# Kernel optimization log

Hardware: AMD Instinct MI355X
Metric: run time of the kernel (lower is better)

## Reference

```python
import jax, jax.numpy as jnp
import numpy as np

DIM = 128
N_VARS = 2048
N_CLAUSES = 8192
N_ROUNDS = 26
ADJ_DENSITY = 0.0015  # ~6 literals per clause


def setup_inputs() -> dict:
    key = jax.random.key(0)
    ks = iter(jax.random.split(key, 40))

    def w(shape):
        fan_in = shape[-1]
        return jax.random.normal(next(ks), shape, jnp.float32) / jnp.sqrt(jnp.float32(fan_in))

    def b(shape):
        return jax.random.normal(next(ks), shape, jnp.float32) * 0.05

    adj = (jax.random.uniform(next(ks), (2 * N_VARS, N_CLAUSES)) < ADJ_DENSITY).astype(jnp.float32)
    inp = {
        'adj': adj,
        'l_init_w': w((DIM, 1)), 'l_init_b': b((DIM,)),
        'c_init_w': w((DIM, 1)), 'c_init_b': b((DIM,)),
        'lmsg_w1': w((DIM, DIM)), 'lmsg_b1': b((DIM,)),
        'lmsg_w2': w((DIM, DIM)), 'lmsg_b2': b((DIM,)),
        'lmsg_w3': w((DIM, DIM)), 'lmsg_b3': b((DIM,)),
        'cmsg_w1': w((DIM, DIM)), 'cmsg_b1': b((DIM,)),
        'cmsg_w2': w((DIM, DIM)), 'cmsg_b2': b((DIM,)),
        'cmsg_w3': w((DIM, DIM)), 'cmsg_b3': b((DIM,)),
        'l_wih': w((4 * DIM, 2 * DIM)), 'l_whh': w((4 * DIM, DIM)),
        'l_bih': b((4 * DIM,)), 'l_bhh': b((4 * DIM,)),
        'c_wih': w((4 * DIM, DIM)), 'c_whh': w((4 * DIM, DIM)),
        'c_bih': b((4 * DIM,)), 'c_bhh': b((4 * DIM,)),
        'lvote_w1': w((DIM, DIM)), 'lvote_b1': b((DIM,)),
        'lvote_w2': w((DIM, DIM)), 'lvote_b2': b((DIM,)),
        'lvote_w3': w((1, DIM)), 'lvote_b3': b((1,)),
    }
    return inp


def _mlp(x, w1, b1, w2, b2, w3, b3):
    x = jax.nn.relu(x @ w1.T + b1)
    x = jax.nn.relu(x @ w2.T + b2)
    return x @ w3.T + b3


def _lstm_step(x, h, c, wih, whh, bih, bhh):
    # torch.nn.LSTM gate order: i, f, g, o
    g = x @ wih.T + h @ whh.T + bih + bhh
    i, f, gg, o = jnp.split(g, 4, axis=-1)
    c = jax.nn.sigmoid(f) * c + jax.nn.sigmoid(i) * jnp.tanh(gg)
    h = jax.nn.sigmoid(o) * jnp.tanh(c)
    return h, c


def reference(adj, l_init_w, l_init_b, c_init_w, c_init_b,
              lmsg_w1, lmsg_b1, lmsg_w2, lmsg_b2, lmsg_w3, lmsg_b3,
              cmsg_w1, cmsg_b1, cmsg_w2, cmsg_b2, cmsg_w3, cmsg_b3,
              l_wih, l_whh, l_bih, l_bhh,
              c_wih, c_whh, c_bih, c_bhh,
              lvote_w1, lvote_b1, lvote_w2, lvote_b2, lvote_w3, lvote_b3):
    n_lits, n_clauses = adj.shape
    n_vars = n_lits // 2
    dim = l_init_b.shape[0]

    # L_init / C_init: Linear(1,dim) applied to ones(1), tiled across rows
    Lh = jnp.broadcast_to(l_init_w[:, 0] + l_init_b, (n_lits, dim))
    Ch = jnp.broadcast_to(c_init_w[:, 0] + c_init_b, (n_clauses, dim))
    Lc = jnp.zeros((n_lits, dim), jnp.float32)
    Cc = jnp.zeros((n_clauses, dim), jnp.float32)

    def step(carry, _):
        Lh, Lc, Ch, Cc = carry
        L_pre = _mlp(Lh, lmsg_w1, lmsg_b1, lmsg_w2, lmsg_b2, lmsg_w3, lmsg_b3)
        LC_msg = adj.T @ L_pre                       # [n_clauses, dim]
        Ch, Cc = _lstm_step(LC_msg, Ch, Cc, c_wih, c_whh, c_bih, c_bhh)
        C_pre = _mlp(Ch, cmsg_w1, cmsg_b1, cmsg_w2, cmsg_b2, cmsg_w3, cmsg_b3)
        CL_msg = adj @ C_pre                         # [2*n_vars, dim]
        L_flip = jnp.concatenate([Lh[n_vars:], Lh[:n_vars]], axis=0)
        x = jnp.concatenate([CL_msg, L_flip], axis=1)  # [2*n_vars, 2*dim]
        Lh, Lc = _lstm_step(x, Lh, Lc, l_wih, l_whh, l_bih, l_bhh)
        return (Lh, Lc, Ch, Cc), None

    (Lh, Lc, Ch, Cc), _ = jax.lax.scan(step, (Lh, Lc, Ch, Cc), None, length=N_ROUNDS)

    logits = Lh
    vote = _mlp(logits, lvote_w1, lvote_b1, lvote_w2, lvote_b2, lvote_w3, lvote_b3)  # [2*n_vars, 1]
    vote_join = jnp.concatenate([vote[:n_vars], vote[n_vars:]], axis=1)  # [n_vars, 2]
    vote_mean = jnp.mean(vote_join)[None]  # single problem in batch -> [1]
    return vote_mean, vote, logits
```

## Files before the change

### kernel.cpp

```cpp
#include <hip/hip_runtime.h>
#include <math.h>

#define NL 4096
#define NV 2048
#define NC 8192
#define DIM 128
#define NG 512
#define NROUNDS 26

#define CSEG 64
#define CSEGLEN 64
#define CSEGCAP 8
#define LSEG 32
#define LSEGLEN 256
#define LSEGCAP 16
#define CCAP 32
#define LCAP 48

__device__ __forceinline__ float sigf(float x){ return 1.0f/(1.0f+expf(-x)); }

__global__ void k_transpose(const float* __restrict__ src, float* __restrict__ dst,
                            int R, int C){
  __shared__ float t[32][33];
  int cb = blockIdx.x*32, rb = blockIdx.y*32;
  int x = threadIdx.x, y = threadIdx.y;
  for (int i = y; i < 32; i += 8){
    int r = rb+i, c = cb+x;
    if (r < R && c < C) t[i][x] = src[(size_t)r*C + c];
  }
  __syncthreads();
  for (int i = y; i < 32; i += 8){
    int c = cb+i, r = rb+x;
    if (c < C && r < R) dst[(size_t)c*R + r] = t[x][i];
  }
}

__global__ void k_permq(const float* __restrict__ W, int K,
                        float* __restrict__ dst, int koff){
  int idx = blockIdx.x*blockDim.x + threadIdx.x;
  if (idx >= K*NG) return;
  int k = idx >> 9, j = idx & (NG-1);
  int g = j & 3, d = j >> 2;
  dst[(size_t)(koff+k)*NG + j] = W[(size_t)(g*DIM+d)*K + k];
}

__global__ void k_permb(const float* __restrict__ bih, const float* __restrict__ bhh,
                        float* __restrict__ bq){
  int j = blockIdx.x*blockDim.x + threadIdx.x;
  if (j >= NG) return;
  int g = j & 3, d = j >> 2;
  bq[j] = bih[g*DIM+d] + bhh[g*DIM+d];
}

__global__ void k_build_cseg(const float* __restrict__ adj,
                             int* __restrict__ scnt, int* __restrict__ slst){
  int idx = blockIdx.x*blockDim.x + threadIdx.x;
  int c4 = idx & (NC/4 - 1);
  int s  = idx >> 11;
  if (s >= CSEG) return;
  int base = s*CSEGLEN;
  int c0 = c4*4;
  int n0=0, n1=0, n2=0, n3=0;
  for (int i = 0; i < CSEGLEN; ++i){
    float4 v = *(const float4*)&adj[(size_t)(base+i)*NC + c0];
    if (v.x != 0.f){ if (n0 < CSEGCAP) slst[((size_t)(c0+0)*CSEG + s)*CSEGCAP + n0] = base+i; ++n0; }
    if (v.y != 0.f){ if (n1 < CSEGCAP) slst[((size_t)(c0+1)*CSEG + s)*CSEGCAP + n1] = base+i; ++n1; }
    if (v.z != 0.f){ if (n2 < CSEGCAP) slst[((size_t)(c0+2)*CSEG + s)*CSEGCAP + n2] = base+i; ++n2; }
    if (v.w != 0.f){ if (n3 < CSEGCAP) slst[((size_t)(c0+3)*CSEG + s)*CSEGCAP + n3] = base+i; ++n3; }
  }
  scnt[(c0+0)*CSEG + s] = n0 < CSEGCAP ? n0 : CSEGCAP;
  scnt[(c0+1)*CSEG + s] = n1 < CSEGCAP ? n1 : CSEGCAP;
  scnt[(c0+2)*CSEG + s] = n2 < CSEGCAP ? n2 : CSEGCAP;
  scnt[(c0+3)*CSEG + s] = n3 < CSEGCAP ? n3 : CSEGCAP;
}

__global__ void k_build_lseg(const float* __restrict__ adj,
                             int* __restrict__ scnt, int* __restrict__ slst){
  int gtid = blockIdx.x*blockDim.x + threadIdx.x;
  int wid  = gtid >> 6;
  int lane = threadIdx.x & 63;
  int l = wid >> 5;
  int s = wid & (LSEG-1);
  if (l >= NL) return;
  int base = s*LSEGLEN;
  int c0 = base + lane*4;
  float4 v = *(const float4*)&adj[(size_t)l*NC + c0];
  float vv[4] = {v.x, v.y, v.z, v.w};
  unsigned long long below = (lane == 0) ? 0ull : ((1ull<<lane)-1ull);
  int* out = slst + ((size_t)l*LSEG + s)*LSEGCAP;
  unsigned long long m[4];
  int nb = 0;
#pragma unroll
  for (int j = 0; j < 4; ++j){
    m[j] = __ballot(vv[j] != 0.f);
    nb += __popcll(m[j] & below);
  }
  int myoff = 0;
#pragma unroll
  for (int j = 0; j < 4; ++j){
    if (vv[j] != 0.f){
      int pos = nb + myoff;
      if (pos < LSEGCAP) out[pos] = c0 + j;
      ++myoff;
    }
  }
  if (lane == 0){
    int tot = 0;
#pragma unroll
    for (int j = 0; j < 4; ++j) tot += __popcll(m[j]);
    scnt[l*LSEG+s] = tot < LSEGCAP ? tot : LSEGCAP;
  }
}

__global__ void k_merge_c(const int* __restrict__ scnt, const int* __restrict__ slst,
                          int* __restrict__ cnt, int* __restrict__ lst){
  int c = blockIdx.x*blockDim.x + threadIdx.x;
  if (c >= NC) return;
  int n = 0;
  for (int s = 0; s < CSEG; ++s){
    int m = scnt[c*CSEG+s];
    const int* in = slst + ((size_t)c*CSEG+s)*CSEGCAP;
    for (int t = 0; t < m; ++t){ if (n < CCAP) lst[(size_t)c*CCAP+n] = in[t]; ++n; }
  }
  cnt[c] = n < CCAP ? n : CCAP;
}

__global__ void k_merge_l(const int* __restrict__ scnt, const int* __restrict__ slst,
                          int* __restrict__ cnt, int* __restrict__ lst){
  int l = blockIdx.x*blockDim.x + threadIdx.x;
  if (l >= NL) return;
  int n = 0;
  for (int s = 0; s < LSEG; ++s){
    int m = scnt[l*LSEG+s];
    const int* in = slst + ((size_t)l*LSEG+s)*LSEGCAP;
    for (int t = 0; t < m; ++t){ if (n < LCAP) lst[(size_t)l*LCAP+n] = in[t]; ++n; }
  }
  cnt[l] = n < LCAP ? n : LCAP;
}

__global__ void k_init(const float* __restrict__ liw, const float* __restrict__ lib,
                       const float* __restrict__ ciw, const float* __restrict__ cib,
                       float* __restrict__ Lh, float* __restrict__ Lc,
                       float* __restrict__ Ch, float* __restrict__ Cc){
  int idx = blockIdx.x*blockDim.x + threadIdx.x;
  int d = idx & (DIM-1);
  if (idx < NL*DIM){ Lh[idx] = liw[d] + lib[d]; Lc[idx] = 0.0f; }
  if (idx < NC*DIM){ Ch[idx] = ciw[d] + cib[d]; Cc[idx] = 0.0f; }
}

template<int CAP>
__global__ __launch_bounds__(256)
void k_gather(const float* __restrict__ X,
              const int* __restrict__ cnt, const int* __restrict__ lst,
              float* __restrict__ out){
  int tid = threadIdx.x;
  int r = blockIdx.x*8 + (tid>>5);
  int q = tid & 31;
  float4 s = make_float4(0.f,0.f,0.f,0.f);
  int n = cnt[r];
  const int* ls = lst + (size_t)r*CAP;
  for (int e = 0; e < n; ++e){
    float4 u = *(const float4*)&X[(size_t)ls[e]*DIM + q*4];
    s.x += u.x; s.y += u.y; s.z += u.z; s.w += u.w;
  }
  *(float4*)&out[(size_t)r*DIM + q*4] = s;
}

template<int ASRC, int BN>
__global__ __launch_bounds__(256)
void k_lstm(const float* __restrict__ Xmsg,
            const float* __restrict__ Hin,
            const float* __restrict__ Wq, const float* __restrict__ bq,
            float* __restrict__ Cst, float* __restrict__ Hout){
  constexpr int KT  = (ASRC==1) ? 256 : 384;
  constexpr int NT  = KT/16;
  constexpr int TN  = BN/16;
  constexpr int BQ  = BN/4;
  constexpr int NBS = (16*BQ)/256;
  __shared__ __align__(16) float As[16][68];
  __shared__ __align__(16) float4 Bs4[16*BQ];
  int tid = threadIdx.x;
  int tx = tid & 15, ty = tid >> 4;
  int m0 = blockIdx.x*64, n0 = blockIdx.y*BN;
  int arow = tid >> 2, akq = tid & 3;
  int grow = m0 + arow;
  int frow = (grow + NV) & (NL-1);

  float acc[4][TN];
#pragma unroll
  for (int r = 0; r < 4; ++r)
#pragma unroll
    for (int c = 0; c < TN; ++c) acc[r][c] = 0.f;

  for (int t = 0; t < NT; ++t){
    int k0 = t*16;
    const float* ap;
    if (ASRC == 1){
      ap = (k0 < 128) ? &Xmsg[(size_t)grow*DIM + k0]
                      : &Hin[(size_t)grow*DIM + (k0-128)];
    } else {
      ap = (k0 < 128) ? &Xmsg[(size_t)grow*DIM + k0]
         : (k0 < 256) ? &Hin[(size_t)frow*DIM + (k0-128)]
                      : &Hin[(size_t)grow*DIM + (k0-256)];
    }
    float4 av = *(const float4*)(ap + akq*4);
    float4 bv[NBS];
#pragma unroll
    for (int i = 0; i < NBS; ++i){
      int s = tid + i*256;
      int bk = s / BQ, bc = s % BQ;
      bv[i] = *(const float4*)&Wq[(size_t)(k0+bk)*NG + n0 + bc*4];
    }
    __syncthreads();
    As[akq*4+0][arow] = av.x;
    As[akq*4+1][arow] = av.y;
    As[akq*4+2][arow] = av.z;
    As[akq*4+3][arow] = av.w;
#pragma unroll
    for (int i = 0; i < NBS; ++i){
      int s = tid + i*256;
      int bk = s / BQ, bc = s % BQ;
      if (BN == 128) Bs4[(bk*2 + (bc&1))*16 + (bc>>1)] = bv[i];
      else           Bs4[bk*16 + bc] = bv[i];
    }
    __syncthreads();
#pragma unroll
    for (int k = 0; k < 16; ++k){
      float4 a = *(const float4*)&As[k][ty*4];
      float ar[4] = {a.x, a.y, a.z, a.w};
      if (TN == 8){
        float4 b0 = Bs4[(k*2+0)*16 + tx];
        float4 b1 = Bs4[(k*2+1)*16 + tx];
        float br[8] = {b0.x,b0.y,b0.z,b0.w,b1.x,b1.y,b1.z,b1.w};
#pragma unroll
        for (int r = 0; r < 4; ++r)
#pragma unroll
          for (int c = 0; c < 8; ++c) acc[r][c] += ar[r]*br[c];
      } else {
        float4 b0 = Bs4[k*16 + tx];
        float br[4] = {b0.x,b0.y,b0.z,b0.w};
#pragma unroll
        for (int r = 0; r < 4; ++r)
#pragma unroll
          for (int c = 0; c < 4; ++c) acc[r][c] += ar[r]*br[c];
      }
    }
  }

  if (TN == 8){
    float4 bq0 = *(const float4*)&bq[n0 + tx*8];
    float4 bq1 = *(const float4*)&bq[n0 + tx*8 + 4];
    int d0 = (n0 >> 2) + tx*2;
#pragma unroll
    for (int rr = 0; rr < 4; ++rr){
      int row = m0 + ty*4 + rr;
      float2 c = *(const float2*)&Cst[(size_t)row*DIM + d0];
      float i0 = acc[rr][0]+bq0.x, f0 = acc[rr][1]+bq0.y;
      float g0 = acc[rr][2]+bq0.z, o0 = acc[rr][3]+bq0.w;
      float i1 = acc[rr][4]+bq1.x, f1 = acc[rr][5]+bq1.y;
      float g1 = acc[rr][6]+bq1.z, o1 = acc[rr][7]+bq1.w;
      float cn0 = sigf(f0)*c.x + sigf(i0)*tanhf(g0);
      float cn1 = sigf(f1)*c.y + sigf(i1)*tanhf(g1);
      float hn0 = sigf(o0)*tanhf(cn0);
      float hn1 = sigf(o1)*tanhf(cn1);
      *(float2*)&Cst[(size_t)row*DIM + d0]  = make_float2(cn0, cn1);
      *(float2*)&Hout[(size_t)row*DIM + d0] = make_float2(hn0, hn1);
    }
  } else {
    float4 bqv = *(const float4*)&bq[n0 + tx*4];
    int d = (n0 >> 2) + tx;
#pragma unroll
    for (int rr = 0; rr < 4; ++rr){
      int row = m0 + ty*4 + rr;
      float c = Cst[(size_t)row*DIM + d];
      float ig = acc[rr][0]+bqv.x, fg = acc[rr][1]+bqv.y;
      float gg = acc[rr][2]+bqv.z, og = acc[rr][3]+bqv.w;
      float cn = sigf(fg)*c + sigf(ig)*tanhf(gg);
      float hn = sigf(og)*tanhf(cn);
      Cst[(size_t)row*DIM + d]  = cn;
      Hout[(size_t)row*DIM + d] = hn;
    }
  }
}

template<int BM>
__global__ __launch_bounds__(256)
void k_mlp3r(const float* __restrict__ in, float* __restrict__ out,
             const float* __restrict__ w1, const float* __restrict__ b1,
             const float* __restrict__ w2, const float* __restrict__ b2,
             const float* __restrict__ w3, const float* __restrict__ b3){
  constexpr int TM = BM/8;
  __shared__ __align__(16) float xs[BM][132];
  __shared__ __align__(16) float4 Bs4[512];
  int tid = threadIdx.x;
  int tx = tid & 31, ty = tid >> 5;
  int m0 = blockIdx.x*BM;
#pragma unroll
  for (int i = 0; i < BM/8; ++i){
    int idx = tid + i*256;
    int row = idx >> 5, c4 = idx & 31;
    *(float4*)&xs[row][c4*4] = *(const float4*)&in[(size_t)(m0+row)*DIM + c4*4];
  }
  const float* W[3] = {w1, w2, w3};
  const float* B[3] = {b1, b2, b3};
#pragma unroll
  for (int l = 0; l < 3; ++l){
    float acc[TM][4];
#pragma unroll
    for (int r = 0; r < TM; ++r)
#pragma unroll
      for (int c = 0; c < 4; ++c) acc[r][c] = 0.f;
    for (int kt = 0; kt < 8; ++kt){
      float4 wv0, wv1;
      { int s = tid;      wv0 = *(const float4*)&W[l][(size_t)(kt*16+(s>>5))*DIM + (s&31)*4]; }
      { int s = tid+256;  wv1 = *(const float4*)&W[l][(size_t)(kt*16+(s>>5))*DIM + (s&31)*4]; }
      __syncthreads();
      { int s = tid;      Bs4[(s>>5)*32 + (s&31)] = wv0; }
      { int s = tid+256;  Bs4[(s>>5)*32 + (s&31)] = wv1; }
      __syncthreads();
#pragma unroll
      for (int k4 = 0; k4 < 4; ++k4){
        float4 a[TM];
#pragma unroll
        for (int r = 0; r < TM; ++r)
          a[r] = *(const float4*)&xs[ty*TM+r][kt*16 + k4*4];
#pragma unroll
        for (int kk = 0; kk < 4; ++kk){
          float4 b = Bs4[(k4*4+kk)*32 + tx];
          float br[4] = {b.x, b.y, b.z, b.w};
#pragma unroll
          for (int r = 0; r < TM; ++r){
            float av = (kk==0) ? a[r].x : (kk==1) ? a[r].y : (kk==2) ? a[r].z : a[r].w;
#pragma unroll
            for (int c = 0; c < 4; ++c) acc[r][c] += av*br[c];
          }
        }
      }
    }
    float4 bb = *(const float4*)&B[l][tx*4];
    if (l < 2){
      __syncthreads();
#pragma unroll
      for (int r = 0; r < TM; ++r){
        float4 v = make_float4(fmaxf(acc[r][0]+bb.x, 0.f), fmaxf(acc[r][1]+bb.y, 0.f),
                               fmaxf(acc[r][2]+bb.z, 0.f), fmaxf(acc[r][3]+bb.w, 0.f));
        *(float4*)&xs[ty*TM+r][tx*4] = v;
      }
    } else {
#pragma unroll
      for (int r = 0; r < TM; ++r){
        int row = m0 + ty*TM + r;
        float4 v = make_float4(acc[r][0]+bb.x, acc[r][1]+bb.y,
                               acc[r][2]+bb.z, acc[r][3]+bb.w);
        *(float4*)&out[(size_t)row*DIM + tx*4] = v;
      }
    }
  }
}

template<bool RELU>
__device__ __forceinline__ void mlp_layer8v(const float (*__restrict__ xs)[DIM],
                                            float (*__restrict__ ys)[DIM],
                                            const float* __restrict__ Wt,
                                            const float* __restrict__ B, int tid){
  int j4 = (tid & 31)*4, slot = tid >> 5;
  float a0=0.f, a1=0.f, a2=0.f, a3=0.f;
#pragma unroll 4
  for (int k = 0; k < DIM; k += 4){
    float4 w0 = *(const float4*)&Wt[(size_t)(k+0)*DIM + j4];
    float4 w1 = *(const float4*)&Wt[(size_t)(k+1)*DIM + j4];
    float4 w2 = *(const float4*)&Wt[(size_t)(k+2)*DIM + j4];
    float4 w3 = *(const float4*)&Wt[(size_t)(k+3)*DIM + j4];
    float4 x  = *(const float4*)&xs[slot][k];
    a0 += x.x*w0.x + x.y*w1.x + x.z*w2.x + x.w*w3.x;
    a1 += x.x*w0.y + x.y*w1.y + x.z*w2.y + x.w*w3.y;
    a2 += x.x*w0.z + x.y*w1.z + x.z*w2.z + x.w*w3.z;
    a3 += x.x*w0.w + x.y*w1.w + x.z*w2.w + x.w*w3.w;
  }
  float4 b = *(const float4*)&B[j4];
  float4 v = make_float4(a0+b.x, a1+b.y, a2+b.z, a3+b.w);
  if (RELU){
    v.x = fmaxf(v.x,0.f); v.y = fmaxf(v.y,0.f);
    v.z = fmaxf(v.z,0.f); v.w = fmaxf(v.w,0.f);
  }
  *(float4*)&ys[slot][j4] = v;
}

__global__ __launch_bounds__(256, 4)
void k_vote(const float* __restrict__ Lh, float* __restrict__ vote,
            float* __restrict__ dout,
            const float* __restrict__ w1t, const float* __restrict__ b1,
            const float* __restrict__ w2t, const float* __restrict__ b2,
            const float* __restrict__ w3, const float* __restrict__ b3){
  __shared__ __align__(16) float xs[8][DIM];
  __shared__ __align__(16) float ys[8][DIM];
  int r0 = blockIdx.x*8;
  int tid = threadIdx.x;
  {
    int row = tid >> 5, c4 = (tid & 31)*4;
    float4 v = *(const float4*)&Lh[(size_t)(r0+row)*DIM + c4];
    *(float4*)&xs[row][c4] = v;
    *(float4*)&dout[1 + NL + (size_t)(r0+row)*DIM + c4] = v;
  }
  __syncthreads();
  mlp_layer8v<true>(xs, ys, w1t, b1, tid);
  __syncthreads();
  mlp_layer8v<true>(ys, xs, w2t, b2, tid);
  __syncthreads();
  int r = tid >> 5, lane32 = tid & 31;
  float4 x = *(const float4*)&xs[r][lane32*4];
  float4 w = *(const float4*)&w3[lane32*4];
  float pp = x.x*w.x + x.y*w.y + x.z*w.z + x.w*w.w;
  pp += __shfl_down(pp, 16, 32);
  pp += __shfl_down(pp, 8, 32);
  pp += __shfl_down(pp, 4, 32);
  pp += __shfl_down(pp, 2, 32);
  pp += __shfl_down(pp, 1, 32);
  if (lane32 == 0){
    float t = pp + b3[0];
    vote[r0+r] = t;
    dout[1 + r0 + r] = t;
  }
}

__global__ void k_mean(const float* __restrict__ vote, float* __restrict__ dout){
  __shared__ float red[256];
  int tid = threadIdx.x;
  float s = 0.f;
  for (int i = tid; i < NL; i += 256) s += vote[i];
  red[tid] = s;
  __syncthreads();
  for (int w = 128; w > 0; w >>= 1){
    if (tid < w) red[tid] += red[tid+w];
    __syncthreads();
  }
  if (tid == 0) dout[0] = red[0] / (float)NL;
}

static inline void launch_transpose(const float* src, float* dst, int R, int C,
                                    hipStream_t stream){
  dim3 g((C+31)/32, (R+31)/32), b(32, 8);
  k_transpose<<<g, b, 0, stream>>>(src, dst, R, C);
}

extern "C" void kernel_launch(void* const* d_in, const int* in_sizes, int n_in,
                              void* d_out, int out_size, void* d_ws, size_t ws_size,
                              hipStream_t stream){
  const float* adj      = (const float*)d_in[0];
  const float* l_init_w = (const float*)d_in[1];
  const float* l_init_b = (const float*)d_in[2];
  const float* c_init_w = (const float*)d_in[3];
  const float* c_init_b = (const float*)d_in[4];
  const float* lmsg_w1  = (const float*)d_in[5];
  const float* lmsg_b1  = (const float*)d_in[6];
  const float* lmsg_w2  = (const float*)d_in[7];
  const float* lmsg_b2  = (const float*)d_in[8];
  const float* lmsg_w3  = (const float*)d_in[9];
  const float* lmsg_b3  = (const float*)d_in[10];
  const float* cmsg_w1  = (const float*)d_in[11];
  const float* cmsg_b1  = (const float*)d_in[12];
  const float* cmsg_w2  = (const float*)d_in[13];
  const float* cmsg_b2  = (const float*)d_in[14];
  const float* cmsg_w3  = (const float*)d_in[15];
  const float* cmsg_b3  = (const float*)d_in[16];
  const float* l_wih    = (const float*)d_in[17];
  const float* l_whh    = (const float*)d_in[18];
  const float* l_bih    = (const float*)d_in[19];
  const float* l_bhh    = (const float*)d_in[20];
  const float* c_wih    = (const float*)d_in[21];
  const float* c_whh    = (const float*)d_in[22];
  const float* c_bih    = (const float*)d_in[23];
  const float* c_bhh    = (const float*)d_in[24];
  const float* lvote_w1 = (const float*)d_in[25];
  const float* lvote_b1 = (const float*)d_in[26];
  const float* lvote_w2 = (const float*)d_in[27];
  const float* lvote_b2 = (const float*)d_in[28];
  const float* lvote_w3 = (const float*)d_in[29];
  const float* lvote_b3 = (const float*)d_in[30];

  char* p = (char*)d_ws;
  auto alloc = [&](size_t bytes) -> void* {
    void* r = (void*)p;
    p += (bytes + 255) & ~(size_t)255;
    return r;
  };
  float* LhA   = (float*)alloc((size_t)NL*DIM*4);
  float* LhB   = (float*)alloc((size_t)NL*DIM*4);
  float* Lc    = (float*)alloc((size_t)NL*DIM*4);
  float* ChA   = (float*)alloc((size_t)NC*DIM*4);
  float* Cc    = (float*)alloc((size_t)NC*DIM*4);
  float* vote  = (float*)alloc((size_t)NL*4);
  int* ccnt    = (int*)alloc((size_t)NC*4);
  int* clst    = (int*)alloc((size_t)NC*CCAP*4);
  int* lcnt    = (int*)alloc((size_t)NL*4);
  int* llst    = (int*)alloc((size_t)NL*LCAP*4);
  float* lm1t  = (float*)alloc((size_t)DIM*DIM*4);
  float* lm2t  = (float*)alloc((size_t)DIM*DIM*4);
  float* lm3t  = (float*)alloc((size_t)DIM*DIM*4);
  float* cm1t  = (float*)alloc((size_t)DIM*DIM*4);
  float* cm2t  = (float*)alloc((size_t)DIM*DIM*4);
  float* cm3t  = (float*)alloc((size_t)DIM*DIM*4);
  float* vw1t  = (float*)alloc((size_t)DIM*DIM*4);
  float* vw2t  = (float*)alloc((size_t)DIM*DIM*4);
  float* WqC   = (float*)alloc((size_t)256*NG*4);
  float* WqL   = (float*)alloc((size_t)384*NG*4);
  float* bqC   = (float*)alloc((size_t)NG*4);
  float* bqL   = (float*)alloc((size_t)NG*4);
  char* scratch = (char*)alloc((size_t)28*1024*1024);
  int* scnt_c  = (int*)scratch;
  int* slst_c  = (int*)(scratch + (size_t)NC*CSEG*4);
  int* scnt_l  = (int*)(scratch + (size_t)(NC*CSEG + NC*CSEG*CSEGCAP)*4);
  int* slst_l  = (int*)(scratch + (size_t)(NC*CSEG + NC*CSEG*CSEGCAP + NL*LSEG)*4);
  float* ChB   = (float*)(scratch);
  float* Cpre  = (float*)(scratch + (size_t)4*1024*1024);
  float* Lpre  = (float*)(scratch + (size_t)8*1024*1024);
  float* Cmsg  = (float*)(scratch + (size_t)10*1024*1024);
  float* Lmsg  = (float*)(scratch + (size_t)14*1024*1024);
  (void)ws_size; (void)in_sizes; (void)n_in; (void)out_size;

  launch_transpose(lmsg_w1, lm1t, DIM, DIM, stream);
  launch_transpose(lmsg_w2, lm2t, DIM, DIM, stream);
  launch_transpose(lmsg_w3, lm3t, DIM, DIM, stream);
  launch_transpose(cmsg_w1, cm1t, DIM, DIM, stream);
  launch_transpose(cmsg_w2, cm2t, DIM, DIM, stream);
  launch_transpose(cmsg_w3, cm3t, DIM, DIM, stream);
  launch_transpose(lvote_w1, vw1t, DIM, DIM, stream);
  launch_transpose(lvote_w2, vw2t, DIM, DIM, stream);
  k_permq<<<(128*NG)/256, 256, 0, stream>>>(c_wih, 128, WqC, 0);
  k_permq<<<(128*NG)/256, 256, 0, stream>>>(c_whh, 128, WqC, 128);
  k_permq<<<(256*NG)/256, 256, 0, stream>>>(l_wih, 256, WqL, 0);
  k_permq<<<(128*NG)/256, 256, 0, stream>>>(l_whh, 128, WqL, 256);
  k_permb<<<NG/256, 256, 0, stream>>>(c_bih, c_bhh, bqC);
  k_permb<<<NG/256, 256, 0, stream>>>(l_bih, l_bhh, bqL);

  k_build_cseg<<<(NC/4)*CSEG/256, 256, 0, stream>>>(adj, scnt_c, slst_c);
  k_build_lseg<<<NL*LSEG*64/256, 256, 0, stream>>>(adj, scnt_l, slst_l);
  k_merge_c<<<NC/256, 256, 0, stream>>>(scnt_c, slst_c, ccnt, clst);
  k_merge_l<<<NL/256, 256, 0, stream>>>(scnt_l, slst_l, lcnt, llst);
  k_init<<<NC*DIM/256, 256, 0, stream>>>(l_init_w, l_init_b, c_init_w, c_init_b,
                                         LhA, Lc, ChA, Cc);

  float* Lh_cur = LhA; float* Lh_nxt = LhB;
  float* Ch_cur = ChA; float* Ch_nxt = ChB;

  k_mlp3r<8><<<NL/8, 256, 0, stream>>>(Lh_cur, Lpre,
                                       lm1t, lmsg_b1, lm2t, lmsg_b2, lm3t, lmsg_b3);
  for (int r = 0; r < NROUNDS; ++r){
    k_gather<CCAP><<<NC/8, 256, 0, stream>>>(Lpre, ccnt, clst, Cmsg);
    k_lstm<1,64><<<dim3(NC/64, 8), 256, 0, stream>>>(Cmsg, Ch_cur, WqC, bqC, Cc, Ch_nxt);
    k_mlp3r<8><<<NC/8, 256, 0, stream>>>(Ch_nxt, Cpre,
                                         cm1t, cmsg_b1, cm2t, cmsg_b2, cm3t, cmsg_b3);
    k_gather<LCAP><<<NL/8, 256, 0, stream>>>(Cpre, lcnt, llst, Lmsg);
    k_lstm<2,64><<<dim3(NL/64, 8), 256, 0, stream>>>(Lmsg, Lh_cur, WqL, bqL, Lc, Lh_nxt);
    k_mlp3r<8><<<NL/8, 256, 0, stream>>>(Lh_nxt, Lpre,
                                         lm1t, lmsg_b1, lm2t, lmsg_b2, lm3t, lmsg_b3);
    float* t;
    t = Lh_cur; Lh_cur = Lh_nxt; Lh_nxt = t;
    t = Ch_cur; Ch_cur = Ch_nxt; Ch_nxt = t;
  }

  k_vote<<<NL/8, 256, 0, stream>>>(Lh_cur, vote, (float*)d_out,
                                   vw1t, lvote_b1, vw2t, lvote_b2,
                                   lvote_w3, lvote_b3);
  k_mean<<<1, 256, 0, stream>>>(vote, (float*)d_out);
}
```

Before: 3.588 ms.

## Fuse sparse neighbor gather into LSTM GEMM kernel prologue

Removes the separate gather kernels and writes the aggregated message rows straight into shared memory at the start of each LSTM GEMM block. The first 128 K-columns then read from that shared tile instead of a global message buffer. This cuts two launches per round and the global write and read of the message tensors. In exchange, each of the 8 column blocks (grid y) repeats the same gather, so sparse reads grow eightfold, and the larger shared tile may reduce occupancy.

```diff
diff --git a/kernel.cpp b/kernel.cpp
--- a/kernel.cpp
+++ b/kernel.cpp
@@ -148,138 +148,104 @@
   if (idx < NC*DIM){ Ch[idx] = ciw[d] + cib[d]; Cc[idx] = 0.0f; }
 }
 
-template<int CAP>
+template<int ASRC>
 __global__ __launch_bounds__(256)
-void k_gather(const float* __restrict__ X,
-              const int* __restrict__ cnt, const int* __restrict__ lst,
-              float* __restrict__ out){
-  int tid = threadIdx.x;
-  int r = blockIdx.x*8 + (tid>>5);
-  int q = tid & 31;
-  float4 s = make_float4(0.f,0.f,0.f,0.f);
-  int n = cnt[r];
-  const int* ls = lst + (size_t)r*CAP;
-  for (int e = 0; e < n; ++e){
-    float4 u = *(const float4*)&X[(size_t)ls[e]*DIM + q*4];
-    s.x += u.x; s.y += u.y; s.z += u.z; s.w += u.w;
-  }
-  *(float4*)&out[(size_t)r*DIM + q*4] = s;
-}
-
-template<int ASRC, int BN>
-__global__ __launch_bounds__(256)
-void k_lstm(const float* __restrict__ Xmsg,
+void k_lstm(const float* __restrict__ Xg,
+            const int* __restrict__ cnt, const int* __restrict__ lst,
             const float* __restrict__ Hin,
             const float* __restrict__ Wq, const float* __restrict__ bq,
             float* __restrict__ Cst, float* __restrict__ Hout){
   constexpr int KT  = (ASRC==1) ? 256 : 384;
   constexpr int NT  = KT/16;
-  constexpr int TN  = BN/16;
-  constexpr int BQ  = BN/4;
-  constexpr int NBS = (16*BQ)/256;
+  constexpr int LCP = (ASRC==1) ? CCAP : LCAP;
+  __shared__ __align__(16) float Am[DIM][68];
   __shared__ __align__(16) float As[16][68];
-  __shared__ __align__(16) float4 Bs4[16*BQ];
+  __shared__ __align__(16) float4 Bs4[16*16];
   int tid = threadIdx.x;
   int tx = tid & 15, ty = tid >> 4;
-  int m0 = blockIdx.x*64, n0 = blockIdx.y*BN;
+  int m0 = blockIdx.x*64, n0 = blockIdx.y*64;
   int arow = tid >> 2, akq = tid & 3;
   int grow = m0 + arow;
   int frow = (grow + NV) & (NL-1);
 
-  float acc[4][TN];
+  {
+    int n = cnt[grow];
+    const int* ls = lst + (size_t)grow*LCP;
+    float4 g[8];
+#pragma unroll
+    for (int j = 0; j < 8; ++j) g[j] = make_float4(0.f,0.f,0.f,0.f);
+    for (int e = 0; e < n; ++e){
+      const float* xr = &Xg[(size_t)ls[e]*DIM];
+#pragma unroll
+      for (int j = 0; j < 8; ++j){
+        float4 u = *(const float4*)&xr[(akq + 4*j)*4];
+        g[j].x += u.x; g[j].y += u.y; g[j].z += u.z; g[j].w += u.w;
+      }
+    }
+#pragma unroll
+    for (int j = 0; j < 8; ++j){
+      int k0 = (akq + 4*j)*4;
+      Am[k0+0][arow] = g[j].x;
+      Am[k0+1][arow] = g[j].y;
+      Am[k0+2][arow] = g[j].z;
+      Am[k0+3][arow] = g[j].w;
+    }
+  }
+  __syncthreads();
+
+  float acc[4][4];
 #pragma unroll
   for (int r = 0; r < 4; ++r)
 #pragma unroll
-    for (int c = 0; c < TN; ++c) acc[r][c] = 0.f;
+    for (int c = 0; c < 4; ++c) acc[r][c] = 0.f;
 
   for (int t = 0; t < NT; ++t){
     int k0 = t*16;
-    const float* ap;
-    if (ASRC == 1){
-      ap = (k0 < 128) ? &Xmsg[(size_t)grow*DIM + k0]
-                      : &Hin[(size_t)grow*DIM + (k0-128)];
+    float4 bv = *(const float4*)&Wq[(size_t)(k0 + (tid>>4))*NG + n0 + (tid&15)*4];
+    if (t >= 8){
+      const float* ap;
+      if (ASRC == 1)       ap = &Hin[(size_t)grow*DIM + (k0-128)];
+      else if (k0 < 256)   ap = &Hin[(size_t)frow*DIM + (k0-128)];
+      else                 ap = &Hin[(size_t)grow*DIM + (k0-256)];
+      float4 av = *(const float4*)(ap + akq*4);
+      __syncthreads();
+      As[akq*4+0][arow] = av.x;
+      As[akq*4+1][arow] = av.y;
+      As[akq*4+2][arow] = av.z;
+      As[akq*4+3][arow] = av.w;
+      Bs4[(tid>>4)*16 + (tid&15)] = bv;
+      __syncthreads();
     } else {
-      ap = (k0 < 128) ? &Xmsg[(size_t)grow*DIM + k0]
-         : (k0 < 256) ? &Hin[(size_t)frow*DIM + (k0-128)]
-                      : &Hin[(size_t)grow*DIM + (k0-256)];
-    }
-    float4 av = *(const float4*)(ap + akq*4);
-    float4 bv[NBS];
-#pragma unroll
-    for (int i = 0; i < NBS; ++i){
-      int s = tid + i*256;
-      int bk = s / BQ, bc = s % BQ;
-      bv[i] = *(const float4*)&Wq[(size_t)(k0+bk)*NG + n0 + bc*4];
-    }
-    __syncthreads();
-    As[akq*4+0][arow] = av.x;
-    As[akq*4+1][arow] = av.y;
-    As[akq*4+2][arow] = av.z;
-    As[akq*4+3][arow] = av.w;
-#pragma unroll
-    for (int i = 0; i < NBS; ++i){
-      int s = tid + i*256;
-      int bk = s / BQ, bc = s % BQ;
-      if (BN == 128) Bs4[(bk*2 + (bc&1))*16 + (bc>>1)] = bv[i];
-      else           Bs4[bk*16 + bc] = bv[i];
-    }
-    __syncthreads();
+      __syncthreads();
+      Bs4[(tid>>4)*16 + (tid&15)] = bv;
+      __syncthreads();
+    }
 #pragma unroll
     for (int k = 0; k < 16; ++k){
-      float4 a = *(const float4*)&As[k][ty*4];
+      float4 a = (t < 8) ? *(const float4*)&Am[k0+k][ty*4]
+                         : *(const float4*)&As[k][ty*4];
       float ar[4] = {a.x, a.y, a.z, a.w};
-      if (TN == 8){
-        float4 b0 = Bs4[(k*2+0)*16 + tx];
-        float4 b1 = Bs4[(k*2+1)*16 + tx];
-        float br[8] = {b0.x,b0.y,b0.z,b0.w,b1.x,b1.y,b1.z,b1.w};
-#pragma unroll
-        for (int r = 0; r < 4; ++r)
-#pragma unroll
-          for (int c = 0; c < 8; ++c) acc[r][c] += ar[r]*br[c];
-      } else {
-        float4 b0 = Bs4[k*16 + tx];
-        float br[4] = {b0.x,b0.y,b0.z,b0.w};
-#pragma unroll
-        for (int r = 0; r < 4; ++r)
-#pragma unroll
-          for (int c = 0; c < 4; ++c) acc[r][c] += ar[r]*br[c];
-      }
-    }
-  }
-
-  if (TN == 8){
-    float4 bq0 = *(const float4*)&bq[n0 + tx*8];
-    float4 bq1 = *(const float4*)&bq[n0 + tx*8 + 4];
-    int d0 = (n0 >> 2) + tx*2;
-#pragma unroll
-    for (int rr = 0; rr < 4; ++rr){
-      int row = m0 + ty*4 + rr;
-      float2 c = *(const float2*)&Cst[(size_t)row*DIM + d0];
-      float i0 = acc[rr][0]+bq0.x, f0 = acc[rr][1]+bq0.y;
-      float g0 = acc[rr][2]+bq0.z, o0 = acc[rr][3]+bq0.w;
-      float i1 = acc[rr][4]+bq1.x, f1 = acc[rr][5]+bq1.y;
-      float g1 = acc[rr][6]+bq1.z, o1 = acc[rr][7]+bq1.w;
-      float cn0 = sigf(f0)*c.x + sigf(i0)*tanhf(g0);
-      float cn1 = sigf(f1)*c.y + sigf(i1)*tanhf(g1);
-      float hn0 = sigf(o0)*tanhf(cn0);
-      float hn1 = sigf(o1)*tanhf(cn1);
-      *(float2*)&Cst[(size_t)row*DIM + d0]  = make_float2(cn0, cn1);
-      *(float2*)&Hout[(size_t)row*DIM + d0] = make_float2(hn0, hn1);
-    }
-  } else {
-    float4 bqv = *(const float4*)&bq[n0 + tx*4];
-    int d = (n0 >> 2) + tx;
-#pragma unroll
-    for (int rr = 0; rr < 4; ++rr){
-      int row = m0 + ty*4 + rr;
-      float c = Cst[(size_t)row*DIM + d];
-      float ig = acc[rr][0]+bqv.x, fg = acc[rr][1]+bqv.y;
-      float gg = acc[rr][2]+bqv.z, og = acc[rr][3]+bqv.w;
-      float cn = sigf(fg)*c + sigf(ig)*tanhf(gg);
-      float hn = sigf(og)*tanhf(cn);
-      Cst[(size_t)row*DIM + d]  = cn;
-      Hout[(size_t)row*DIM + d] = hn;
-    }
+      float4 b0 = Bs4[k*16 + tx];
+      float br[4] = {b0.x, b0.y, b0.z, b0.w};
+#pragma unroll
+      for (int r = 0; r < 4; ++r)
+#pragma unroll
+        for (int c = 0; c < 4; ++c) acc[r][c] += ar[r]*br[c];
+    }
+  }
+
+  float4 bqv = *(const float4*)&bq[n0 + tx*4];
+  int d = (n0 >> 2) + tx;
+#pragma unroll
+  for (int rr = 0; rr < 4; ++rr){
+    int row = m0 + ty*4 + rr;
+    float c = Cst[(size_t)row*DIM + d];
+    float ig = acc[rr][0]+bqv.x, fg = acc[rr][1]+bqv.y;
+    float gg = acc[rr][2]+bqv.z, og = acc[rr][3]+bqv.w;
+    float cn = sigf(fg)*c + sigf(ig)*tanhf(gg);
+    float hn = sigf(og)*tanhf(cn);
+    Cst[(size_t)row*DIM + d]  = cn;
+    Hout[(size_t)row*DIM + d] = hn;
   }
 }
 
@@ -514,8 +480,6 @@
   float* ChB   = (float*)(scratch);
   float* Cpre  = (float*)(scratch + (size_t)4*1024*1024);
   float* Lpre  = (float*)(scratch + (size_t)8*1024*1024);
-  float* Cmsg  = (float*)(scratch + (size_t)10*1024*1024);
-  float* Lmsg  = (float*)(scratch + (size_t)14*1024*1024);
   (void)ws_size; (void)in_sizes; (void)n_in; (void)out_size;
 
   launch_transpose(lmsg_w1, lm1t, DIM, DIM, stream);
@@ -546,12 +510,12 @@
   k_mlp3r<8><<<NL/8, 256, 0, stream>>>(Lh_cur, Lpre,
                                        lm1t, lmsg_b1, lm2t, lmsg_b2, lm3t, lmsg_b3);
   for (int r = 0; r < NROUNDS; ++r){
-    k_gather<CCAP><<<NC/8, 256, 0, stream>>>(Lpre, ccnt, clst, Cmsg);
-    k_lstm<1,64><<<dim3(NC/64, 8), 256, 0, stream>>>(Cmsg, Ch_cur, WqC, bqC, Cc, Ch_nxt);
+    k_lstm<1><<<dim3(NC/64, 8), 256, 0, stream>>>(
+        Lpre, ccnt, clst, Ch_cur, WqC, bqC, Cc, Ch_nxt);
     k_mlp3r<8><<<NC/8, 256, 0, stream>>>(Ch_nxt, Cpre,
                                          cm1t, cmsg_b1, cm2t, cmsg_b2, cm3t, cmsg_b3);
-    k_gather<LCAP><<<NL/8, 256, 0, stream>>>(Cpre, lcnt, llst, Lmsg);
-    k_lstm<2,64><<<dim3(NL/64, 8), 256, 0, stream>>>(Lmsg, Lh_cur, WqL, bqL, Lc, Lh_nxt);
+    k_lstm<2><<<dim3(NL/64, 8), 256, 0, stream>>>(
+        Cpre, lcnt, llst, Lh_cur, WqL, bqL, Lc, Lh_nxt);
     k_mlp3r<8><<<NL/8, 256, 0, stream>>>(Lh_nxt, Lpre,
                                          lm1t, lmsg_b1, lm2t, lmsg_b2, lm3t, lmsg_b3);
     float* t;
```

Measured after the change: 3.872 ms. 7.9% more time.
